# Kernel tuning notes

Measured on AMD Instinct MI355X. Metric: run time of the kernel, lower is better.

The kernel has to match this reference:

```python
import jax, jax.numpy as jnp
import numpy as np

N_NODES = 50000
N_EDGES = 800000
IN_DIM = 128
HID = 64
N_LAYERS = 3


def setup_inputs() -> dict:
    key = jax.random.key(0)
    ks = jax.random.split(key, 12)
    x = jax.random.normal(ks[0], (N_NODES, IN_DIM), dtype=jnp.float32)
    edge_index = jax.random.randint(ks[1], (2, N_EDGES), 0, N_NODES, dtype=jnp.int64)
    s = 0.05
    Wp = jax.random.normal(ks[2], (IN_DIM, HID), dtype=jnp.float32) * s
    bp = jax.random.normal(ks[3], (HID,), dtype=jnp.float32) * s
    # per-layer EdgeConv MLP params, stacked over layers
    W1 = jax.random.normal(ks[4], (N_LAYERS, 2 * HID, HID), dtype=jnp.float32) * s
    b1 = jax.random.normal(ks[5], (N_LAYERS, HID), dtype=jnp.float32) * s
    W2 = jax.random.normal(ks[6], (N_LAYERS, HID, HID), dtype=jnp.float32) * s
    b2 = jax.random.normal(ks[7], (N_LAYERS, HID), dtype=jnp.float32) * s
    Wo = jax.random.normal(ks[8], (HID, 1), dtype=jnp.float32) * s
    bo = jax.random.normal(ks[9], (1,), dtype=jnp.float32) * s
    return {"x": x, "edge_index": edge_index, "Wp": Wp, "bp": bp,
            "W1": W1, "b1": b1, "W2": W2, "b2": b2, "Wo": Wo, "bo": bo}


def _edge_conv(h, src, dst, W1, b1, W2, b2):
    # PyG EdgeConv: message = MLP(cat[x_i, x_j - x_i]), aggr = max over incoming edges
    xi = h[dst]                       # [E, H] center (target) features
    xj = h[src]                       # [E, H] neighbor (source) features
    e = jnp.concatenate([xi, xj - xi], axis=-1)   # [E, 2H]
    m = jnp.maximum(e @ W1 + b1, 0.0) @ W2 + b2   # [E, H]
    agg = jax.ops.segment_max(m, dst, num_segments=N_NODES)  # [N, H]
    # nodes with no incoming edges get 0 (PyG scatter-max fill value)
    return jnp.where(jnp.isfinite(agg), agg, 0.0)


def reference(x, edge_index, Wp, bp, W1, b1, W2, b2, Wo, bo):
    src, dst = edge_index[0], edge_index[1]
    h = x @ Wp + bp                   # input projection [N, H]
    for l in range(N_LAYERS):
        residual = h
        h = _edge_conv(h, src, dst, W1[l], b1[l], W2[l], b2[l])
        h = jnp.maximum(h, 0.0)       # relu; dropout is identity in eval
        h = h + residual
    return (h @ Wo + bo)[:, 0]        # squeeze(-1) -> [N]
```

## Files before the change

### kernel.cpp

```cpp
#include <hip/hip_runtime.h>

#define NN 50000
#define IN_DIM 128
#define HID 64
#define NLAYERS 3
#define NB 1563
#define CH 128
#define NPART 8
#define BPP 196
#define PQ_BLOCKS 782

typedef __attribute__((ext_vector_type(8))) _Float16 f16x8;
typedef __attribute__((ext_vector_type(2))) _Float16 f16x2;
typedef __attribute__((ext_vector_type(4))) float f32x4;

__device__ __forceinline__ unsigned pkh(float a, float b) {
    return __builtin_bit_cast(unsigned, __builtin_amdgcn_cvt_pkrtz(a, b));
}
__device__ __forceinline__ unsigned short f2h(float f) {
    f16x2 v = __builtin_bit_cast(f16x2, __builtin_amdgcn_cvt_pkrtz(f, 0.f));
    return __builtin_bit_cast(short2, v).x;
}
__device__ __forceinline__ float h2f(unsigned short u) {
    return (float)__builtin_bit_cast(_Float16, u);
}

__device__ __forceinline__ unsigned addrelu2(unsigned q, unsigned p) {
    f16x2 qq = __builtin_bit_cast(f16x2, q);
    f16x2 pp = __builtin_bit_cast(f16x2, p);
    f16x2 s = qq + pp;
    f16x2 z = {(_Float16)0.f, (_Float16)0.f};
    f16x2 r = __builtin_elementwise_max(s, z);
    return __builtin_bit_cast(unsigned, r);
}


__global__ void __launch_bounds__(256) k_hist(const int* __restrict__ dst,
                                              int* __restrict__ cntc, int E, int CE) {
    __shared__ int lh[NB];
    int g = blockIdx.x;
    for (int i = threadIdx.x; i < NB; i += 256) lh[i] = 0;
    __syncthreads();
    int e0 = g * CE, e1 = min(E, e0 + CE);
    for (int e = e0 + threadIdx.x; e < e1; e += 256) atomicAdd(&lh[dst[e] >> 5], 1);
    __syncthreads();
    for (int i = threadIdx.x; i < NB; i += 256) cntc[g * NB + i] = lh[i];
}

__global__ void k_base(const int* __restrict__ cntc, int* __restrict__ basec,
                       int* __restrict__ bincnt) {
    int b = blockIdx.x * 256 + threadIdx.x;
    if (b < NB) {
        int run = 0;
        for (int g = 0; g < CH; g++) {
            basec[g * NB + b] = run;
            run += cntc[g * NB + b];
        }
        bincnt[b] = run;
    }
}

__global__ void k_binscan(const int* __restrict__ bincnt, int* __restrict__ binoff) {
    __shared__ int s[256];
    int t = threadIdx.x;
    int carry = 0;
    for (int c0 = 0; c0 < NB; c0 += 256) {
        int v = (c0 + t < NB) ? bincnt[c0 + t] : 0;
        s[t] = v;
        __syncthreads();
        for (int d = 1; d < 256; d <<= 1) {
            int a = (t >= d) ? s[t - d] : 0;
            __syncthreads();
            s[t] += a;
            __syncthreads();
        }
        if (c0 + t < NB) binoff[c0 + t] = carry + s[t] - v;
        carry += s[255];
        __syncthreads();
    }
}

__global__ void __launch_bounds__(256) k_scatter(
    const int* __restrict__ src, const int* __restrict__ dst,
    const int* __restrict__ basec, const int* __restrict__ binoff,
    unsigned* __restrict__ bscratch, int E, int CE) {
    __shared__ int cur[BPP];
    int p = blockIdx.x & (NPART - 1);
    int g = blockIdx.x >> 3;
    int blo = p * BPP, bhi = min(NB, blo + BPP);
    for (int i = threadIdx.x; i < bhi - blo; i += 256) {
        int b = blo + i;
        cur[i] = binoff[b] + basec[g * NB + b];
    }
    __syncthreads();
    int e0 = g * CE, e1 = min(E, e0 + CE);
    for (int e = e0 + threadIdx.x; e < e1; e += 256) {
        int d = dst[e];
        int bin = d >> 5;
        if (bin >= blo && bin < bhi) {
            int pos = atomicAdd(&cur[bin - blo], 1);
            bscratch[pos] = ((unsigned)(d & 31) << 16) | (unsigned)src[e];
        }
    }
}

__global__ void __launch_bounds__(256) k_binsort(
    const unsigned* __restrict__ bscratch, const int* __restrict__ bincnt,
    const int* __restrict__ binoff, unsigned short* __restrict__ csr,
    int2* __restrict__ meta) {
    __shared__ unsigned entries[1024];
    __shared__ unsigned short sorted[1024];
    __shared__ int cnt[32];
    int bin = blockIdx.x, t = threadIdx.x;
    int n = bincnt[bin], boff = binoff[bin];
    for (int i = t; i < n; i += 256) entries[i] = bscratch[boff + i];
    if (t < 32) cnt[t] = 0;
    __syncthreads();
    for (int i = t; i < n; i += 256) atomicAdd(&cnt[entries[i] >> 16], 1);
    __syncthreads();
    if (t < 32) {
        int c = cnt[t];
        int s = c;
#pragma unroll
        for (int d = 1; d < 32; d <<= 1) {
            int o = __shfl_up(s, d, 64);
            if (t >= d) s += o;
        }
        int node = bin * 32 + t;
        if (node < NN) meta[node] = make_int2(boff + s - c, c);
        cnt[t] = s - c;
    }
    __syncthreads();
    for (int i = t; i < n; i += 256) {
        unsigned e = entries[i];
        int p = atomicAdd(&cnt[e >> 16], 1);
        sorted[p] = (unsigned short)(e & 0xffffu);
    }
    __syncthreads();
    for (int i = t; i < n; i += 256) csr[boff + i] = sorted[i];
}


__global__ void __launch_bounds__(256) k_projpq(
    const float* __restrict__ x, const float* __restrict__ Wp,
    const float* __restrict__ bp, const float* __restrict__ W1,
    const float* __restrict__ b1, unsigned short* __restrict__ h,
    unsigned short* __restrict__ P, unsigned short* __restrict__ Qb) {
    __shared__ float hs[4][16][66];
    int lane = threadIdx.x & 63, wave = threadIdx.x >> 6;
    int col = lane & 15, quad = lane >> 4;
    int node0 = (blockIdx.x * 4 + wave) * 16;
    if (node0 >= NN) return;

    f16x8 bw[4][4];
#pragma unroll
    for (int t = 0; t < 4; t++)
#pragma unroll
        for (int kc = 0; kc < 4; kc++) {
            uint4 u;
#pragma unroll
            for (int jp = 0; jp < 4; jp++) {
                int k0 = kc * 32 + quad * 8 + jp * 2;
                ((unsigned*)&u)[jp] = pkh(Wp[k0 * HID + t * 16 + col],
                                          Wp[(k0 + 1) * HID + t * 16 + col]);
            }
            bw[t][kc] = __builtin_bit_cast(f16x8, u);
        }
    const float4* xr = (const float4*)(x + (size_t)(node0 + col) * IN_DIM);
    f16x8 ax[4];
#pragma unroll
    for (int kc = 0; kc < 4; kc++) {
        float4 f0 = xr[kc * 8 + quad * 2], f1 = xr[kc * 8 + quad * 2 + 1];
        uint4 u;
        u.x = pkh(f0.x, f0.y); u.y = pkh(f0.z, f0.w);
        u.z = pkh(f1.x, f1.y); u.w = pkh(f1.z, f1.w);
        ax[kc] = __builtin_bit_cast(f16x8, u);
    }
#pragma unroll
    for (int t = 0; t < 4; t++) {
        f32x4 c = (f32x4)(0.f);
#pragma unroll
        for (int kc = 0; kc < 4; kc++)
            c = __builtin_amdgcn_mfma_f32_16x16x32_f16(ax[kc], bw[t][kc], c, 0, 0, 0);
        float bv = bp[t * 16 + col];
#pragma unroll
        for (int r = 0; r < 4; r++) {
            float hv = c[r] + bv;
            int row = quad * 4 + r;
            h[(size_t)(node0 + row) * HID + t * 16 + col] = f2h(hv);
            hs[wave][row][t * 16 + col] = hv;
        }
    }

    f16x8 bfr[8][2];
#pragma unroll
    for (int t = 0; t < 8; t++)
#pragma unroll
        for (int hf = 0; hf < 2; hf++) {
            uint4 u;
#pragma unroll
            for (int jp = 0; jp < 4; jp++) {
                int k0 = hf * 32 + quad * 8 + jp * 2;
                float w0, w1v;
                if (t < 4) {
                    int n = t * 16 + col;
                    w0  = W1[k0 * HID + n] - W1[(HID + k0) * HID + n];
                    w1v = W1[(k0 + 1) * HID + n] - W1[(HID + k0 + 1) * HID + n];
                } else {
                    int n = (t - 4) * 16 + col;
                    w0  = W1[(HID + k0) * HID + n];
                    w1v = W1[(HID + k0 + 1) * HID + n];
                }
                ((unsigned*)&u)[jp] = pkh(w0, w1v);
            }
            bfr[t][hf] = __builtin_bit_cast(f16x8, u);
        }
    const float* hl = &hs[wave][col][0];
    uint4 au, bu;
    {
        float2 e0 = *(const float2*)(hl + quad * 8);
        float2 e1 = *(const float2*)(hl + quad * 8 + 2);
        float2 e2 = *(const float2*)(hl + quad * 8 + 4);
        float2 e3 = *(const float2*)(hl + quad * 8 + 6);
        au.x = pkh(e0.x, e0.y); au.y = pkh(e1.x, e1.y);
        au.z = pkh(e2.x, e2.y); au.w = pkh(e3.x, e3.y);
        float2 f0 = *(const float2*)(hl + 32 + quad * 8);
        float2 f1 = *(const float2*)(hl + 32 + quad * 8 + 2);
        float2 f2 = *(const float2*)(hl + 32 + quad * 8 + 4);
        float2 f3 = *(const float2*)(hl + 32 + quad * 8 + 6);
        bu.x = pkh(f0.x, f0.y); bu.y = pkh(f1.x, f1.y);
        bu.z = pkh(f2.x, f2.y); bu.w = pkh(f3.x, f3.y);
    }
    f16x8 a0 = __builtin_bit_cast(f16x8, au);
    f16x8 a1 = __builtin_bit_cast(f16x8, bu);
#pragma unroll
    for (int t = 0; t < 8; t++) {
        f32x4 c = __builtin_amdgcn_mfma_f32_16x16x32_f16(a0, bfr[t][0], (f32x4)(0.f), 0, 0, 0);
        c = __builtin_amdgcn_mfma_f32_16x16x32_f16(a1, bfr[t][1], c, 0, 0, 0);
        if (t < 4) {
            float bv = b1[t * 16 + col];
#pragma unroll
            for (int r = 0; r < 4; r++)
                P[(size_t)(node0 + quad * 4 + r) * HID + t * 16 + col] = f2h(c[r] + bv);
        } else {
#pragma unroll
            for (int r = 0; r < 4; r++)
                Qb[(size_t)(node0 + quad * 4 + r) * HID + (t - 4) * 16 + col] = f2h(c[r]);
        }
    }
}

__global__ void __launch_bounds__(256) k_pq_mfma(
    const unsigned short* __restrict__ h, const float* __restrict__ W1,
    const float* __restrict__ b1, unsigned short* __restrict__ P,
    unsigned short* __restrict__ Qb, int layer) {
    int lane = threadIdx.x & 63, wave = threadIdx.x >> 6;
    int col = lane & 15, quad = lane >> 4;
    int node0 = (blockIdx.x * 4 + wave) * 16;
    if (node0 >= NN) return;
    const float* W1l = W1 + layer * 2 * HID * HID;

    f16x8 bfr[8][2];
#pragma unroll
    for (int t = 0; t < 8; t++)
#pragma unroll
        for (int hf = 0; hf < 2; hf++) {
            uint4 u;
#pragma unroll
            for (int jp = 0; jp < 4; jp++) {
                int k0 = hf * 32 + quad * 8 + jp * 2;
                float w0, w1v;
                if (t < 4) {
                    int n = t * 16 + col;
                    w0  = W1l[k0 * HID + n] - W1l[(HID + k0) * HID + n];
                    w1v = W1l[(k0 + 1) * HID + n] - W1l[(HID + k0 + 1) * HID + n];
                } else {
                    int n = (t - 4) * 16 + col;
                    w0  = W1l[(HID + k0) * HID + n];
                    w1v = W1l[(HID + k0 + 1) * HID + n];
                }
                ((unsigned*)&u)[jp] = pkh(w0, w1v);
            }
            bfr[t][hf] = __builtin_bit_cast(f16x8, u);
        }

    const uint4* hrow = (const uint4*)(h + (size_t)(node0 + col) * HID);
    uint4 au = hrow[quad];
    uint4 bu = hrow[4 + quad];
    f16x8 a0 = __builtin_bit_cast(f16x8, au);
    f16x8 a1 = __builtin_bit_cast(f16x8, bu);

#pragma unroll
    for (int t = 0; t < 8; t++) {
        f32x4 c = __builtin_amdgcn_mfma_f32_16x16x32_f16(a0, bfr[t][0], (f32x4)(0.f), 0, 0, 0);
        c = __builtin_amdgcn_mfma_f32_16x16x32_f16(a1, bfr[t][1], c, 0, 0, 0);
        if (t < 4) {
            float bv = b1[layer * HID + t * 16 + col];
#pragma unroll
            for (int r = 0; r < 4; r++)
                P[(size_t)(node0 + quad * 4 + r) * HID + t * 16 + col] = f2h(c[r] + bv);
        } else {
#pragma unroll
            for (int r = 0; r < 4; r++)
                Qb[(size_t)(node0 + quad * 4 + r) * HID + (t - 4) * 16 + col] = f2h(c[r]);
        }
    }
}

__global__ void __launch_bounds__(256) k_edge(
    const unsigned short* __restrict__ P, const unsigned short* __restrict__ Qb,
    const float* __restrict__ W2, const float* __restrict__ b2,
    const int2* __restrict__ meta, const unsigned short* __restrict__ csr,
    unsigned short* __restrict__ h, int layer, int nw,
    int fin, const float* __restrict__ Wo, const float* __restrict__ bo,
    float* __restrict__ outp) {
    int lane = threadIdx.x & 63;
    int col = lane & 15, quad = lane >> 4;
    int wid = (blockIdx.x * blockDim.x + threadIdx.x) >> 6;

    const float* W2l = W2 + layer * HID * HID;
    f16x8 bfr[4][2];
#pragma unroll
    for (int t = 0; t < 4; t++)
#pragma unroll
        for (int hf = 0; hf < 2; hf++) {
            uint4 u;
#pragma unroll
            for (int jp = 0; jp < 4; jp++) {
                int k0 = hf * 32 + quad * 8 + jp * 2;
                ((unsigned*)&u)[jp] = pkh(W2l[k0 * HID + t * 16 + col],
                                          W2l[(k0 + 1) * HID + t * 16 + col]);
            }
            bfr[t][hf] = __builtin_bit_cast(f16x8, u);
        }
    float b2v = b2[layer * HID + lane];
    float wov = fin ? Wo[lane] : 0.f;

    if (wid >= NN) return;
    int2 md = meta[wid];
    unsigned short hres = h[(size_t)wid * HID + lane];

    for (int node = wid; node < NN; node += nw) {
        int pf = (node + nw < NN) ? node + nw : node;
        int2 nmd = meta[pf];
        unsigned short nhres = h[(size_t)pf * HID + lane];

        int start = __builtin_amdgcn_readfirstlane(md.x);
        int cnt   = __builtin_amdgcn_readfirstlane(md.y);
        float res = h2f(hres);
        float outv = 0.f;
        if (cnt > 0) {
            const uint4* prow = (const uint4*)(P + (size_t)node * HID);
            uint4 p0 = prow[quad];
            uint4 p1 = prow[4 + quad];
            f32x4 mx[4];
#pragma unroll
            for (int t = 0; t < 4; t++) mx[t] = (f32x4)(-3.4e38f);
            int nbatch = (cnt + 15) >> 4;
            int s = csr[start + (col < cnt ? col : 0)];
            const uint4* qr = (const uint4*)(Qb + (size_t)s * HID);
            uint4 q0 = qr[quad], q1 = qr[4 + quad];
            for (int b = 0; b < nbatch; b++) {
                uint4 nq0, nq1;
                if (b + 1 < nbatch) {
                    int b0 = (b + 1) * 16;
                    int idx = b0 + col;
                    int s2 = csr[start + (idx < cnt ? idx : b0)];
                    const uint4* qr2 = (const uint4*)(Qb + (size_t)s2 * HID);
                    nq0 = qr2[quad];
                    nq1 = qr2[4 + quad];
                }
                uint4 a0u, a1u;
                a0u.x = addrelu2(q0.x, p0.x);
                a0u.y = addrelu2(q0.y, p0.y);
                a0u.z = addrelu2(q0.z, p0.z);
                a0u.w = addrelu2(q0.w, p0.w);
                a1u.x = addrelu2(q1.x, p1.x);
                a1u.y = addrelu2(q1.y, p1.y);
                a1u.z = addrelu2(q1.z, p1.z);
                a1u.w = addrelu2(q1.w, p1.w);
                f16x8 a0 = __builtin_bit_cast(f16x8, a0u);
                f16x8 a1 = __builtin_bit_cast(f16x8, a1u);
#pragma unroll
                for (int t = 0; t < 4; t++) {
                    f32x4 c = __builtin_amdgcn_mfma_f32_16x16x32_f16(
                        a0, bfr[t][0], (f32x4)(0.f), 0, 0, 0);
                    c = __builtin_amdgcn_mfma_f32_16x16x32_f16(
                        a1, bfr[t][1], c, 0, 0, 0);
#pragma unroll
                    for (int r = 0; r < 4; r++)
                        mx[t][r] = fmaxf(mx[t][r], c[r]);
                }
                q0 = nq0;
                q1 = nq1;
            }
            float v[4];
#pragma unroll
            for (int t = 0; t < 4; t++) {
                v[t] = fmaxf(fmaxf(mx[t][0], mx[t][1]), fmaxf(mx[t][2], mx[t][3]));
                v[t] = fmaxf(v[t], __shfl_xor(v[t], 16, 64));
                v[t] = fmaxf(v[t], __shfl_xor(v[t], 32, 64));
            }
            float vs = quad == 0 ? v[0] : quad == 1 ? v[1] : quad == 2 ? v[2] : v[3];
            outv = fmaxf(vs + b2v, 0.f);
        }
        float hv = outv + res;
        h[(size_t)node * HID + lane] = f2h(hv);
        if (fin) {
            float v = hv * wov;
#pragma unroll
            for (int m = 32; m >= 1; m >>= 1) v += __shfl_xor(v, m, 64);
            if (lane == 0) outp[node] = v + bo[0];
        }
        md = nmd;
        hres = nhres;
    }
}

extern "C" void kernel_launch(void* const* d_in, const int* in_sizes, int n_in,
                              void* d_out, int out_size, void* d_ws, size_t ws_size,
                              hipStream_t stream) {
    const float* x  = (const float*)d_in[0];
    const int*   ei = (const int*)d_in[1];
    const float* Wp = (const float*)d_in[2];
    const float* bp = (const float*)d_in[3];
    const float* W1 = (const float*)d_in[4];
    const float* b1 = (const float*)d_in[5];
    const float* W2 = (const float*)d_in[6];
    const float* b2 = (const float*)d_in[7];
    const float* Wo = (const float*)d_in[8];
    const float* bo = (const float*)d_in[9];
    float* out = (float*)d_out;

    const int E = in_sizes[1] / 2;
    const int N = NN;
    const int* srcp = ei;
    const int* dstp = ei + E;

    unsigned short* h  = (unsigned short*)d_ws;
    unsigned short* Pb = h + (size_t)N * HID;
    unsigned short* Qb = Pb + (size_t)N * HID;
    int* cntc   = (int*)(Qb + (size_t)N * HID);
    int* basec  = cntc + CH * NB;
    int* bincnt = basec + CH * NB;
    int* binoff = bincnt + NB;
    int2* meta  = (int2*)(binoff + NB);
    unsigned* bscratch = (unsigned*)(meta + N);
    unsigned short* csr = (unsigned short*)(bscratch + E);

    const int CE = (E + CH - 1) / CH;

    k_hist<<<CH, 256, 0, stream>>>(dstp, cntc, E, CE);
    k_base<<<(NB + 255) / 256, 256, 0, stream>>>(cntc, basec, bincnt);
    k_binscan<<<1, 256, 0, stream>>>(bincnt, binoff);
    k_scatter<<<CH * NPART, 256, 0, stream>>>(srcp, dstp, basec, binoff, bscratch, E, CE);
    k_binsort<<<NB, 256, 0, stream>>>(bscratch, bincnt, binoff, csr, meta);

    k_projpq<<<PQ_BLOCKS, 256, 0, stream>>>(x, Wp, bp, W1, b1, h, Pb, Qb);

    const int EDGE_BLOCKS = 2048;
    const int NW = EDGE_BLOCKS * 256 / 64;
    for (int l = 0; l < NLAYERS; l++) {
        if (l > 0)
            k_pq_mfma<<<PQ_BLOCKS, 256, 0, stream>>>(h, W1, b1, Pb, Qb, l);
        k_edge<<<EDGE_BLOCKS, 256, 0, stream>>>(Pb, Qb, W2, b2, meta, csr, h, l, NW,
                                                l == NLAYERS - 1 ? 1 : 0, Wo, bo, out);
    }
}
```

Baseline: 292.2 us.

## Fuse histogram into projection kernel and coalesce neighbor gathers via LDS

Runs the dst-histogram blocks as extra blocks of the input-projection kernel, removing a separate launch and letting both overlap. In the edge kernel, each group of 8 lanes now loads a full contiguous neighbor Q row, which is then transposed through per-wave LDS staging into the MFMA operand layout. This aims for better-coalesced gathers at the cost of extra LDS stores and loads per batch.

```diff
diff --git a/kernel.cpp b/kernel.cpp
--- a/kernel.cpp
+++ b/kernel.cpp
@@ -34,18 +34,6 @@
     return __builtin_bit_cast(unsigned, r);
 }
 
-
-__global__ void __launch_bounds__(256) k_hist(const int* __restrict__ dst,
-                                              int* __restrict__ cntc, int E, int CE) {
-    __shared__ int lh[NB];
-    int g = blockIdx.x;
-    for (int i = threadIdx.x; i < NB; i += 256) lh[i] = 0;
-    __syncthreads();
-    int e0 = g * CE, e1 = min(E, e0 + CE);
-    for (int e = e0 + threadIdx.x; e < e1; e += 256) atomicAdd(&lh[dst[e] >> 5], 1);
-    __syncthreads();
-    for (int i = threadIdx.x; i < NB; i += 256) cntc[g * NB + i] = lh[i];
-}
 
 __global__ void k_base(const int* __restrict__ cntc, int* __restrict__ basec,
                        int* __restrict__ bincnt) {
@@ -140,13 +128,27 @@
     for (int i = t; i < n; i += 256) csr[boff + i] = sorted[i];
 }
 
-
-__global__ void __launch_bounds__(256) k_projpq(
+__global__ void __launch_bounds__(256) k_front(
     const float* __restrict__ x, const float* __restrict__ Wp,
     const float* __restrict__ bp, const float* __restrict__ W1,
     const float* __restrict__ b1, unsigned short* __restrict__ h,
-    unsigned short* __restrict__ P, unsigned short* __restrict__ Qb) {
-    __shared__ float hs[4][16][66];
+    unsigned short* __restrict__ P, unsigned short* __restrict__ Qb,
+    const int* __restrict__ dst, int* __restrict__ cntc, int E, int CE) {
+    __shared__ char smraw[4 * 16 * 66 * 4];
+
+    if (blockIdx.x >= PQ_BLOCKS) {
+        int* lh = (int*)smraw;
+        int g = blockIdx.x - PQ_BLOCKS;
+        for (int i = threadIdx.x; i < NB; i += 256) lh[i] = 0;
+        __syncthreads();
+        int e0 = g * CE, e1 = min(E, e0 + CE);
+        for (int e = e0 + threadIdx.x; e < e1; e += 256) atomicAdd(&lh[dst[e] >> 5], 1);
+        __syncthreads();
+        for (int i = threadIdx.x; i < NB; i += 256) cntc[g * NB + i] = lh[i];
+        return;
+    }
+
+    float (*hs)[16][66] = (float (*)[16][66])smraw;
     int lane = threadIdx.x & 63, wave = threadIdx.x >> 6;
     int col = lane & 15, quad = lane >> 4;
     int node0 = (blockIdx.x * 4 + wave) * 16;
@@ -314,8 +316,11 @@
     unsigned short* __restrict__ h, int layer, int nw,
     int fin, const float* __restrict__ Wo, const float* __restrict__ bo,
     float* __restrict__ outp) {
+    __shared__ uint4 qstage[4][16][9];
     int lane = threadIdx.x & 63;
     int col = lane & 15, quad = lane >> 4;
+    int wave = threadIdx.x >> 6;
+    int rrow = lane >> 3, sseg = lane & 7;
     int wid = (blockIdx.x * blockDim.x + threadIdx.x) >> 6;
 
     const float* W2l = W2 + layer * HID * HID;
@@ -357,19 +362,27 @@
 #pragma unroll
             for (int t = 0; t < 4; t++) mx[t] = (f32x4)(-3.4e38f);
             int nbatch = (cnt + 15) >> 4;
-            int s = csr[start + (col < cnt ? col : 0)];
-            const uint4* qr = (const uint4*)(Qb + (size_t)s * HID);
-            uint4 q0 = qr[quad], q1 = qr[4 + quad];
+            uint4 v1, v2;
+            {
+                int e1 = rrow, e2 = 8 + rrow;
+                int s1 = csr[start + (e1 < cnt ? e1 : 0)];
+                int s2 = csr[start + (e2 < cnt ? e2 : 0)];
+                v1 = ((const uint4*)(Qb + (size_t)s1 * HID))[sseg];
+                v2 = ((const uint4*)(Qb + (size_t)s2 * HID))[sseg];
+            }
             for (int b = 0; b < nbatch; b++) {
-                uint4 nq0, nq1;
+                qstage[wave][rrow][sseg] = v1;
+                qstage[wave][8 + rrow][sseg] = v2;
                 if (b + 1 < nbatch) {
                     int b0 = (b + 1) * 16;
-                    int idx = b0 + col;
-                    int s2 = csr[start + (idx < cnt ? idx : b0)];
-                    const uint4* qr2 = (const uint4*)(Qb + (size_t)s2 * HID);
-                    nq0 = qr2[quad];
-                    nq1 = qr2[4 + quad];
+                    int e1 = b0 + rrow, e2 = b0 + 8 + rrow;
+                    int s1 = csr[start + (e1 < cnt ? e1 : b0)];
+                    int s2 = csr[start + (e2 < cnt ? e2 : b0)];
+                    v1 = ((const uint4*)(Qb + (size_t)s1 * HID))[sseg];
+                    v2 = ((const uint4*)(Qb + (size_t)s2 * HID))[sseg];
                 }
+                uint4 q0 = qstage[wave][col][quad];
+                uint4 q1 = qstage[wave][col][4 + quad];
                 uint4 a0u, a1u;
                 a0u.x = addrelu2(q0.x, p0.x);
                 a0u.y = addrelu2(q0.y, p0.y);
@@ -391,8 +404,6 @@
                     for (int r = 0; r < 4; r++)
                         mx[t][r] = fmaxf(mx[t][r], c[r]);
                 }
-                q0 = nq0;
-                q1 = nq1;
             }
             float v[4];
 #pragma unroll
@@ -450,13 +461,12 @@
 
     const int CE = (E + CH - 1) / CH;
 
-    k_hist<<<CH, 256, 0, stream>>>(dstp, cntc, E, CE);
+    k_front<<<PQ_BLOCKS + CH, 256, 0, stream>>>(x, Wp, bp, W1, b1, h, Pb, Qb,
+                                                dstp, cntc, E, CE);
     k_base<<<(NB + 255) / 256, 256, 0, stream>>>(cntc, basec, bincnt);
     k_binscan<<<1, 256, 0, stream>>>(bincnt, binoff);
     k_scatter<<<CH * NPART, 256, 0, stream>>>(srcp, dstp, basec, binoff, bscratch, E, CE);
     k_binsort<<<NB, 256, 0, stream>>>(bscratch, bincnt, binoff, csr, meta);
-
-    k_projpq<<<PQ_BLOCKS, 256, 0, stream>>>(x, Wp, bp, W1, b1, h, Pb, Qb);
 
     const int EDGE_BLOCKS = 2048;
     const int NW = EDGE_BLOCKS * 256 / 64;
```

Measured after the change: 281.8 us. 3.6% less time.
